# Kernel tuning notes

Hardware: AMD Instinct MI355X
Metric: run time of the kernel (lower is better)

The kernel has to match this reference:

```python
import jax, jax.numpy as jnp
import numpy as np

B, U, HEADS, S = 16, 1024, 8, 1024


def setup_inputs() -> dict:
    key = jax.random.key(0)
    k1, k2, k3, k4 = jax.random.split(key, 4)
    x = jax.random.normal(k1, (B, U, S), dtype=jnp.float32)
    mask = jax.random.randint(k2, (B, S, S), 0, 2).astype(bool)
    w_qkv = jax.random.normal(k3, (3 * U, U), dtype=jnp.float32) * 0.02
    w_out = jax.random.normal(k4, (U, U), dtype=jnp.float32) * 0.02
    return {"x": x, "mask": mask, "w_qkv": w_qkv, "w_out": w_out}


def reference(x, mask, w_qkv, w_out):
    # x: (B, U, S), mask: (B, n_queries, n_keys) bool
    b, u, s = x.shape
    h = HEADS
    c = u // h  # head (chunk) size
    scale = 1.0 / np.sqrt(c).astype(np.float32)

    # 1x1-conv QKV projection (bias=False): (3U, U) x (B, U, S) -> (B, 3U, S)
    qkv = jnp.einsum('ou,bus->bos', w_qkv, x)
    Q, K, V = jnp.split(qkv, 3, axis=1)           # each (B, U, S)
    Qh = Q.reshape(b, h, c, s)
    Kh = K.reshape(b, h, c, s)
    Vh = V.reshape(b, h, c, s)

    # attention logits: (B, H, n_q, n_k)
    A = jnp.einsum('bhcq,bhck->bhqk', Qh, Kh)

    # relu activation with per-query valid-key-count normalization
    m = mask.sum(axis=2)[:, :, None]              # (B, n_q, 1) count of valid keys
    n_elem = jnp.where(mask, m, 1).astype(A.dtype)[:, None]  # (B, 1, n_q, n_k)
    mask_b = mask[:, None]                        # broadcast over heads
    A = jnp.where(mask_b, jax.nn.relu(A) * scale, -jnp.inf)
    A = A / n_elem
    A = jnp.where(jnp.isinf(A), jnp.zeros((), A.dtype), A)

    # attention-value aggregation (faithful math of broadcast+sum): (B, H, C, n_q)
    Ch = jnp.einsum('bhqk,bhck->bhcq', A, Vh)
    Cc = Ch.reshape(b, u, s)

    # finishing 1x1-conv linear layer
    return jnp.einsum('ou,bus->bos', w_out, Cc)
```

## Files before the change

### kernel.cpp

```cpp
#include <hip/hip_runtime.h>

#define B_DIM 16
#define U_DIM 1024
#define H_DIM 8
#define S_DIM 1024
#define C_DIM 128
#define KD 1024
#define SCALE 0.08838834764831845f

typedef __attribute__((ext_vector_type(8))) short s16x8;
typedef __attribute__((ext_vector_type(4))) float f32x4;

__device__ __forceinline__ void gll16(const void* g, void* l) {
  __builtin_amdgcn_global_load_lds(
      (const __attribute__((address_space(1))) unsigned int*)g,
      (__attribute__((address_space(3))) unsigned int*)l, 16, 0, 0);
}
__device__ __forceinline__ unsigned short f2bf(float f) {
  unsigned u = __float_as_uint(f);
  u += 0x7FFF + ((u >> 16) & 1u);
  return (unsigned short)(u >> 16);
}
#define MFMA16(a, b, c) __builtin_amdgcn_mfma_f32_16x16x32_bf16(a, b, c, 0, 0, 0)

__global__ void detect_mask(const unsigned char* __restrict__ mask_raw, int* __restrict__ flag) {
  __shared__ int not01, notf;
  if (threadIdx.x == 0) { not01 = 0; notf = 0; }
  __syncthreads();
  const unsigned int* p = (const unsigned int*)mask_raw;
  int l01 = 0, lf = 0;
  for (int i = threadIdx.x; i < 4096; i += 256) {
    unsigned int v = p[i];
    if (v != 0u && v != 1u) l01 = 1;
    if (v != 0u && v != 0x3F800000u) lf = 1;
  }
  if (l01) atomicOr(&not01, 1);
  if (lf) atomicOr(&notf, 1);
  __syncthreads();
  if (threadIdx.x == 0) flag[0] = (!not01) ? 0 : ((!notf) ? 2 : 1);
}

__global__ __launch_bounds__(256) void pack_mask(const unsigned char* __restrict__ mask_raw,
                                                 const int* __restrict__ flag,
                                                 unsigned long long* __restrict__ bits) {
  __shared__ unsigned char tile[64][80];
  const int t = threadIdx.x;
  const int kt = blockIdx.x * 64, qw = blockIdx.y, b = blockIdx.z;
  const int mk = flag[0];
  const int q = t >> 2, kbase = (t & 3) * 16;
  const size_t row = (size_t)(b * S_DIM + qw * 64 + q);
  if (mk == 1) {
    uint4 v = *(const uint4*)(mask_raw + (row << 10) + kt + kbase);
    *(uint4*)&tile[q][kbase] = v;
  } else if (mk == 0) {
    const int* p = (const int*)mask_raw + (row << 10) + kt + kbase;
#pragma unroll
    for (int j = 0; j < 4; ++j) {
      int4 v = ((const int4*)p)[j];
      uchar4 o;
      o.x = v.x ? 1 : 0; o.y = v.y ? 1 : 0; o.z = v.z ? 1 : 0; o.w = v.w ? 1 : 0;
      *(uchar4*)&tile[q][kbase + j * 4] = o;
    }
  } else {
    const float* p = (const float*)mask_raw + (row << 10) + kt + kbase;
#pragma unroll
    for (int j = 0; j < 4; ++j) {
      float4 v = ((const float4*)p)[j];
      uchar4 o;
      o.x = (v.x != 0.f) ? 1 : 0; o.y = (v.y != 0.f) ? 1 : 0;
      o.z = (v.z != 0.f) ? 1 : 0; o.w = (v.w != 0.f) ? 1 : 0;
      *(uchar4*)&tile[q][kbase + j * 4] = o;
    }
  }
  __syncthreads();
  const int wave = t >> 6, lane = t & 63;
#pragma unroll
  for (int qq = 0; qq < 16; ++qq) {
    int qr = wave * 16 + qq;
    unsigned long long bal = __ballot(tile[qr][lane] != 0);
    if (lane == 0)
      bits[(size_t)blockIdx.x * (B_DIM * S_DIM) + (size_t)b * S_DIM + qw * 64 + qr] = bal;
  }
}

__global__ __launch_bounds__(256) void invm_from_bits(const unsigned long long* __restrict__ bits,
                                                      float* __restrict__ invm) {
  int idx = blockIdx.x * 256 + threadIdx.x;
  int s = 0;
#pragma unroll
  for (int kt = 0; kt < S_DIM / 64; ++kt)
    s += __popcll(bits[(size_t)kt * (B_DIM * S_DIM) + idx]);
  invm[idx] = (s > 0) ? (SCALE / (float)s) : 0.f;
}

__global__ __launch_bounds__(256) void cvt_bf16(const float* __restrict__ in,
                                                unsigned short* __restrict__ out, int n) {
  int i = (blockIdx.x * 256 + threadIdx.x) * 4;
  if (i < n) {
    float4 v = *(const float4*)(in + i);
    ushort4 o;
    o.x = f2bf(v.x); o.y = f2bf(v.y); o.z = f2bf(v.z); o.w = f2bf(v.w);
    *(ushort4*)(out + i) = o;
  }
}

__global__ __launch_bounds__(256) void transpose_x(const float* __restrict__ x,
                                                   unsigned short* __restrict__ xT) {
  __shared__ float T[32][33];
  const int t = threadIdx.x, r = t >> 3, c4 = (t & 7) * 4;
  const int s0 = blockIdx.x * 32, u0 = blockIdx.y * 32;
  const size_t base = (size_t)blockIdx.z * U_DIM * S_DIM;
  float4 v = *(const float4*)(x + base + (size_t)(u0 + r) * S_DIM + s0 + c4);
  T[r][c4 + 0] = v.x; T[r][c4 + 1] = v.y; T[r][c4 + 2] = v.z; T[r][c4 + 3] = v.w;
  __syncthreads();
  ushort4 o;
  o.x = f2bf(T[c4 + 0][r]); o.y = f2bf(T[c4 + 1][r]);
  o.z = f2bf(T[c4 + 2][r]); o.w = f2bf(T[c4 + 3][r]);
  *(ushort4*)(xT + base + (size_t)(s0 + r) * U_DIM + u0 + c4) = o;
}

__global__ __launch_bounds__(256) void transpose_v(const unsigned short* __restrict__ qkvT,
                                                   unsigned short* __restrict__ VT) {
  __shared__ unsigned short T[32][34];
  const int t = threadIdx.x, r = t >> 3, c4 = (t & 7) * 4;
  const int k0 = blockIdx.x * 32, c0 = blockIdx.y * 32;
  const unsigned short* qb = qkvT + (size_t)blockIdx.z * S_DIM * (3 * U_DIM);
  ushort4 v = *(const ushort4*)(qb + (size_t)(k0 + r) * (3 * U_DIM) + 2 * U_DIM + c0 + c4);
  T[r][c4 + 0] = v.x; T[r][c4 + 1] = v.y; T[r][c4 + 2] = v.z; T[r][c4 + 3] = v.w;
  __syncthreads();
  ushort4 o;
  o.x = T[c4 + 0][r]; o.y = T[c4 + 1][r]; o.z = T[c4 + 2][r]; o.w = T[c4 + 3][r];
  *(ushort4*)(VT + (size_t)blockIdx.z * U_DIM * S_DIM + (size_t)(c0 + r) * S_DIM + k0 + c4) = o;
}

template <typename OUT>
__global__ __launch_bounds__(512, 2) void gemm256(const unsigned short* __restrict__ A,
                                                  const unsigned short* __restrict__ Bm,
                                                  OUT* __restrict__ D,
                                                  long long sAb, long long sBb, long long sDb,
                                                  int N) {
  __shared__ unsigned short sA0[256 * 64], sB0[256 * 64];
  __shared__ unsigned short sA1[256 * 64], sB1[256 * 64];
  const int tid = threadIdx.x;
  const int wave = tid >> 6, lane = tid & 63;
  const int l15 = lane & 15, quad = lane >> 4;
  const int wm = wave & 3, wn = wave >> 2;
  const unsigned int Lb = blockIdx.x + gridDim.x * (blockIdx.y + gridDim.y * blockIdx.z);
  const unsigned int nwg = gridDim.x * gridDim.y * gridDim.z;
  const unsigned int logical = (Lb & 7u) * (nwg >> 3) + (Lb >> 3);
  const int bx = logical % gridDim.x;
  const unsigned int rem = logical / gridDim.x;
  const int by = rem % gridDim.y;
  const int bz = rem / gridDim.y;
  const int m0 = by * 256, n0 = bx * 256;
  A += (size_t)bz * sAb + (size_t)m0 * KD;
  Bm += (size_t)bz * sBb + (size_t)n0 * KD;
  D += (size_t)bz * sDb;

  const int r0 = tid >> 3;
  const int kc0 = (tid & 7) ^ (r0 & 7);
  const unsigned short* pA = A + (size_t)r0 * KD + kc0 * 8;
  const unsigned short* pB = Bm + (size_t)r0 * KD + kc0 * 8;
  const int wo = wave * 512;

#define STG_U0(SA, K0)                                        \
  do {                                                        \
    gll16(pA + (K0), &(SA)[wo]);                              \
    gll16(pA + 64 * KD + (K0), &(SA)[4096 + wo]);             \
  } while (0)
#define STG_U1(SA, K0)                                        \
  do {                                                        \
    gll16(pA + 128 * KD + (K0), &(SA)[8192 + wo]);            \
    gll16(pA + 192 * KD + (K0), &(SA)[12288 + wo]);           \
  } while (0)
#define STG_U2(SB, K0)                                        \
  do {                                                        \
    gll16(pB + (K0), &(SB)[wo]);                              \
    gll16(pB + 128 * KD + (K0), &(SB)[8192 + wo]);            \
  } while (0)
#define STG_U3(SB, K0)                                        \
  do {                                                        \
    gll16(pB + 64 * KD + (K0), &(SB)[4096 + wo]);             \
    gll16(pB + 192 * KD + (K0), &(SB)[12288 + wo]);           \
  } while (0)

#define WAITB(VN)                                             \
  do {                                                        \
    asm volatile("s_waitcnt vmcnt(" #VN ")" ::: "memory");    \
    __builtin_amdgcn_s_barrier();                             \
    asm volatile("" ::: "memory");                            \
  } while (0)

  s16x8 a[4][2];
  f32x4 acc[4][8] = {};

#define LDA(SA)                                                                         \
  do {                                                                                  \
    _Pragma("unroll") for (int i = 0; i < 4; ++i) {                                     \
      int row = wm * 64 + i * 16 + l15;                                                 \
      _Pragma("unroll") for (int ks = 0; ks < 2; ++ks)                                  \
          a[i][ks] = *(const s16x8*)&(SA)[row * 64 + (((ks * 4 + quad) ^ (row & 7)) * 8)]; \
    }                                                                                   \
  } while (0)

#define PHASE(SB, P)                                                                    \
  do {                                                                                  \
    s16x8 b[2][2];                                                                      \
    _Pragma("unroll") for (int jj = 0; jj < 2; ++jj) {                                  \
      int row = wn * 128 + ((P) * 2 + jj) * 16 + l15;                                   \
      _Pragma("unroll") for (int ks = 0; ks < 2; ++ks)                                  \
          b[jj][ks] = *(const s16x8*)&(SB)[row * 64 + (((ks * 4 + quad) ^ (row & 7)) * 8)]; \
    }                                                                                   \
    __builtin_amdgcn_s_setprio(1);                                                      \
    _Pragma("unroll") for (int ks = 0; ks < 2; ++ks)                                    \
        _Pragma("unroll") for (int i = 0; i < 4; ++i)                                   \
            _Pragma("unroll") for (int jj = 0; jj < 2; ++jj)                            \
                acc[i][(P) * 2 + jj] = MFMA16(a[i][ks], b[jj][ks], acc[i][(P) * 2 + jj]); \
    __builtin_amdgcn_s_setprio(0);                                                      \
  } while (0)

#define TILE(SA, SB, SAn, SBn, K1)                            \
  do {                                                        \
    WAITB(2);                                                 \
    STG_U0(SAn, K1);                                          \
    LDA(SA);                                                  \
    PHASE(SB, 0);                                             \
    STG_U1(SAn, K1);                                          \
    PHASE(SB, 1);                                             \
    WAITB(4);                                                 \
    STG_U2(SBn, K1);                                          \
    PHASE(SB, 2);                                             \
    STG_U3(SBn, K1);                                          \
    PHASE(SB, 3);                                             \
  } while (0)

#define TILE_LAST(CA, CB)                                     \
  do {                                                        \
    WAITB(2);                                                 \
    LDA(CA);                                                  \
    PHASE(CB, 0);                                             \
    PHASE(CB, 1);                                             \
    WAITB(0);                                                 \
    PHASE(CB, 2);                                             \
    PHASE(CB, 3);                                             \
  } while (0)

  STG_U0(sA0, 0); STG_U1(sA0, 0); STG_U2(sB0, 0); STG_U3(sB0, 0);

  for (int kt = 0; kt < 14; kt += 2) {
    TILE(sA0, sB0, sA1, sB1, (kt + 1) * 64);
    TILE(sA1, sB1, sA0, sB0, (kt + 2) * 64);
  }
  TILE(sA0, sB0, sA1, sB1, 15 * 64);
  TILE_LAST(sA1, sB1);
#undef TILE
#undef TILE_LAST
#undef PHASE
#undef LDA
#undef WAITB
#undef STG_U0
#undef STG_U1
#undef STG_U2
#undef STG_U3

#pragma unroll
  for (int i = 0; i < 4; ++i)
#pragma unroll
    for (int j = 0; j < 8; ++j) {
      f32x4 v = acc[i][j];
#pragma unroll
      for (int r = 0; r < 4; ++r) {
        int m = m0 + wm * 64 + i * 16 + quad * 4 + r;
        int n = n0 + wn * 128 + j * 16 + l15;
        if constexpr (sizeof(OUT) == 2) D[(size_t)m * N + n] = f2bf(v[r]);
        else D[(size_t)m * N + n] = v[r];
      }
    }
}

__global__ __launch_bounds__(512, 2) void attn_mfma(const unsigned short* __restrict__ qkvT,
                                                    const unsigned short* __restrict__ VT,
                                                    const unsigned long long* __restrict__ bits,
                                                    const float* __restrict__ invm,
                                                    unsigned short* __restrict__ CcT, int b0) {
  __shared__ unsigned short QV[128 * 128];
  __shared__ unsigned short Ks[64 * 128];
  __shared__ unsigned short Vs[128 * 64];
  __shared__ unsigned short Ps[128 * 64];

  const int tid = threadIdx.x, wave = tid >> 6, lane = tid & 63;
  const int l15 = lane & 15, quad = lane >> 4;
  const int qhalf = wave >> 2, kw = wave & 3;
  const int L = blockIdx.x + 8 * (blockIdx.y + 8 * blockIdx.z);
  const int cpx = (8 * H_DIM * gridDim.z) >> 3;
  const int logical = (L & 7) * cpx + (L >> 3);
  const int qt = logical & 7, h = (logical >> 3) & 7, z = logical >> 6;
  const int q0 = qt * 128, b = b0 + z;
  const unsigned short* qB = qkvT + (size_t)z * S_DIM * (3 * U_DIM);
  const unsigned short* Vb = VT + (size_t)z * U_DIM * S_DIM + (size_t)h * C_DIM * S_DIM;

#pragma unroll
  for (int pp = 0; pp < 4; ++pp) {
    int p = pp * 512 + tid;
    int row = p >> 4, c = (p & 15) ^ (row & 7);
    gll16(qB + (size_t)(q0 + row) * (3 * U_DIM) + h * C_DIM + c * 8, &QV[p * 8]);
  }
#pragma unroll
  for (int pp = 0; pp < 2; ++pp) {
    int p = pp * 512 + tid;
    int row = p >> 4, c = (p & 15) ^ (row & 7);
    gll16(qB + (size_t)row * (3 * U_DIM) + U_DIM + h * C_DIM + c * 8, &Ks[p * 8]);
    int vrow = p >> 3, vkc = (p & 7) ^ (vrow & 7);
    gll16(Vb + (size_t)vrow * S_DIM + vkc * 8, &Vs[p * 8]);
  }
  __syncthreads();

  s16x8 qf[4][4];
#pragma unroll
  for (int j = 0; j < 4; ++j)
#pragma unroll
    for (int kk = 0; kk < 4; ++kk) {
      int row = qhalf * 64 + j * 16 + l15;
      qf[j][kk] = *(const s16x8*)&QV[row * 128 + ((kk * 4 + quad) ^ (row & 7)) * 8];
    }
  float invf[4];
  {
    const float* ivp = invm + (size_t)b * S_DIM + q0 + qhalf * 64;
#pragma unroll
    for (int j = 0; j < 4; ++j) invf[j] = ivp[j * 16 + l15];
  }
  __syncthreads();

  f32x4 pacc[4][2] = {};

  for (int kt = 0; kt < S_DIM / 64; ++kt) {
    if (kt < S_DIM / 64 - 1) {
      const int kn = (kt + 1) * 64;
      unsigned short* vdst = (kt & 1) ? Vs : QV;
#pragma unroll
      for (int pp = 0; pp < 2; ++pp) {
        int p = pp * 512 + tid;
        int vrow = p >> 3, vkc = (p & 7) ^ (vrow & 7);
        gll16(Vb + (size_t)vrow * S_DIM + kn + vkc * 8, &vdst[p * 8]);
      }
    }

    unsigned long long w64[4];
    {
      const unsigned long long* mw =
          bits + (size_t)kt * (B_DIM * S_DIM) + (size_t)b * S_DIM + q0 + qhalf * 64;
#pragma unroll
      for (int j = 0; j < 4; ++j) w64[j] = mw[j * 16 + l15];
    }

    s16x8 af[4];
#pragma unroll
    for (int kk = 0; kk < 4; ++kk) {
      int row = kw * 16 + l15;
      af[kk] = *(const s16x8*)&Ks[row * 128 + ((kk * 4 + quad) ^ (row & 7)) * 8];
    }
    f32x4 sacc[4] = {};
    __builtin_amdgcn_s_setprio(1);
#pragma unroll
    for (int kk = 0; kk < 4; ++kk)
#pragma unroll
      for (int j = 0; j < 4; ++j) sacc[j] = MFMA16(af[kk], qf[j][kk], sacc[j]);
    __builtin_amdgcn_s_setprio(0);

#pragma unroll
    for (int j = 0; j < 4; ++j) {
      const unsigned int m4 = (unsigned int)(w64[j] >> (kw * 16 + quad * 4)) & 0xFu;
      float p[4];
#pragma unroll
      for (int r = 0; r < 4; ++r) {
        float t = fmaxf(sacc[j][r], 0.f) * invf[j];
        p[r] = ((m4 >> r) & 1u) ? t : 0.f;
      }
      unsigned int pk0, pk1;
      asm("v_cvt_pk_bf16_f32 %0, %1, %2" : "=v"(pk0) : "v"(p[0]), "v"(p[1]));
      asm("v_cvt_pk_bf16_f32 %0, %1, %2" : "=v"(pk1) : "v"(p[2]), "v"(p[3]));
      int q = qhalf * 64 + j * 16 + l15;
      int chunk = (kw * 2 + (quad >> 1)) ^ (q & 7);
      *(uint2*)&Ps[q * 64 + chunk * 8 + (quad & 1) * 4] = make_uint2(pk0, pk1);
    }
    __syncthreads();

    if (kt < S_DIM / 64 - 1) {
      const int kn = (kt + 1) * 64;
#pragma unroll
      for (int pp = 0; pp < 2; ++pp) {
        int p = pp * 512 + tid;
        int row = p >> 4, c = (p & 15) ^ (row & 7);
        gll16(qB + (size_t)(kn + row) * (3 * U_DIM) + U_DIM + h * C_DIM + c * 8, &Ks[p * 8]);
      }
    }

    const unsigned short* vbuf = (kt & 1) ? QV : Vs;
#pragma unroll
    for (int ks = 0; ks < 2; ++ks) {
      s16x8 pf[4], vf[2];
#pragma unroll
      for (int i = 0; i < 4; ++i) {
        int row = qhalf * 64 + i * 16 + l15;
        pf[i] = *(const s16x8*)&Ps[row * 64 + ((ks * 4 + quad) ^ (row & 7)) * 8];
      }
#pragma unroll
      for (int j = 0; j < 2; ++j) {
        int row = kw * 32 + j * 16 + l15;
        vf[j] = *(const s16x8*)&vbuf[row * 64 + ((ks * 4 + quad) ^ (row & 7)) * 8];
      }
      __builtin_amdgcn_s_setprio(1);
#pragma unroll
      for (int i = 0; i < 4; ++i)
#pragma unroll
        for (int j = 0; j < 2; ++j) pacc[i][j] = MFMA16(pf[i], vf[j], pacc[i][j]);
      __builtin_amdgcn_s_setprio(0);
    }
    __syncthreads();
  }

  unsigned short* cb = CcT + (size_t)z * S_DIM * U_DIM;
#pragma unroll
  for (int i = 0; i < 4; ++i)
#pragma unroll
    for (int j = 0; j < 2; ++j) {
      f32x4 v = pacc[i][j];
#pragma unroll
      for (int r = 0; r < 4; ++r) {
        int q = q0 + qhalf * 64 + i * 16 + quad * 4 + r;
        int c = h * C_DIM + kw * 32 + j * 16 + l15;
        cb[(size_t)q * U_DIM + c] = f2bf(v[r]);
      }
    }
}

extern "C" void kernel_launch(void* const* d_in, const int* in_sizes, int n_in,
                              void* d_out, int out_size, void* d_ws, size_t ws_size,
                              hipStream_t stream) {
  const float* x = (const float*)d_in[0];
  const unsigned char* mask_raw = (const unsigned char*)d_in[1];
  const float* w_qkv = (const float*)d_in[2];
  const float* w_out = (const float*)d_in[3];
  float* out = (float*)d_out;

  char* ws = (char*)d_ws;
  int* flag = (int*)ws;
  float* invm = (float*)(ws + 256);
  unsigned long long* bits = (unsigned long long*)(ws + 256 + 65536);
  unsigned short* wqkv_bf = (unsigned short*)((char*)bits + (size_t)B_DIM * S_DIM * 16 * 8);
  unsigned short* wout_bf = (unsigned short*)((char*)wqkv_bf + (size_t)3 * U_DIM * U_DIM * 2);
  char* heap = (char*)wout_bf + (size_t)U_DIM * U_DIM * 2;

  const size_t xT_pb = (size_t)U_DIM * S_DIM * 2;
  const size_t qkvT_pb = (size_t)3 * U_DIM * S_DIM * 2;
  const size_t vT_pb = (size_t)U_DIM * S_DIM * 2;
  const size_t ccT_pb = (size_t)U_DIM * S_DIM * 2;
  const size_t per_batch = xT_pb + qkvT_pb + vT_pb + ccT_pb;
  const size_t fixed = (size_t)(heap - ws);
  int nb = (ws_size > fixed) ? (int)((ws_size - fixed) / per_batch) : 1;
  if (nb < 1) nb = 1;
  if (nb > B_DIM) nb = B_DIM;

  unsigned short* xT = (unsigned short*)heap;
  unsigned short* qkvT = (unsigned short*)(heap + (size_t)nb * xT_pb);
  unsigned short* VT = (unsigned short*)(heap + (size_t)nb * (xT_pb + qkvT_pb));
  unsigned short* CcT = (unsigned short*)(heap + (size_t)nb * (xT_pb + qkvT_pb + vT_pb));

  detect_mask<<<1, 256, 0, stream>>>(mask_raw, flag);
  pack_mask<<<dim3(S_DIM / 64, S_DIM / 64, B_DIM), 256, 0, stream>>>(mask_raw, flag, bits);
  invm_from_bits<<<(B_DIM * S_DIM) / 256, 256, 0, stream>>>(bits, invm);
  cvt_bf16<<<(3 * U_DIM * U_DIM) / 1024, 256, 0, stream>>>(w_qkv, wqkv_bf, 3 * U_DIM * U_DIM);
  cvt_bf16<<<(U_DIM * U_DIM) / 1024, 256, 0, stream>>>(w_out, wout_bf, U_DIM * U_DIM);

  for (int b0 = 0; b0 < B_DIM; b0 += nb) {
    int cnt = (B_DIM - b0 < nb) ? (B_DIM - b0) : nb;
    transpose_x<<<dim3(S_DIM / 32, U_DIM / 32, cnt), 256, 0, stream>>>(
        x + (size_t)b0 * U_DIM * S_DIM, xT);
    gemm256<unsigned short><<<dim3(3 * U_DIM / 256, S_DIM / 256, cnt), 512, 0, stream>>>(
        xT, wqkv_bf, qkvT, (long long)U_DIM * S_DIM, 0LL, (long long)3 * U_DIM * S_DIM, 3 * U_DIM);
    transpose_v<<<dim3(S_DIM / 32, U_DIM / 32, cnt), 256, 0, stream>>>(qkvT, VT);
    attn_mfma<<<dim3(S_DIM / 128, H_DIM, cnt), 512, 0, stream>>>(
        qkvT, VT, bits, invm, CcT, b0);
    gemm256<float><<<dim3(S_DIM / 256, U_DIM / 256, cnt), 512, 0, stream>>>(
        wout_bf, CcT, out + (size_t)b0 * U_DIM * S_DIM, 0LL,
        (long long)U_DIM * S_DIM, (long long)U_DIM * S_DIM, S_DIM);
  }
}
```

Baseline: 462.8 us.

## Double-buffer K tiles and use 1024-thread attention blocks with one barrier per step

The attention kernel now runs 16 waves per block instead of 8, each covering 32 queries, which shrinks per-wave accumulators and registers. K tiles get a second LDS buffer, so the next K and V tiles are prefetched at the top of each step, and the mid-step barrier becomes a raw s_barrier after an lgkmcnt wait. Q is staged in two halves through a smaller buffer to fit in LDS. Dropping the vmcnt wait before the raw barrier risks reading stale Vs/Ks if global-to-LDS loads have not landed, since only the loop-end __syncthreads waits on them.

```diff
diff --git a/kernel.cpp b/kernel.cpp
--- a/kernel.cpp
+++ b/kernel.cpp
@@ -278,19 +278,20 @@
     }
 }
 
-__global__ __launch_bounds__(512, 2) void attn_mfma(const unsigned short* __restrict__ qkvT,
-                                                    const unsigned short* __restrict__ VT,
-                                                    const unsigned long long* __restrict__ bits,
-                                                    const float* __restrict__ invm,
-                                                    unsigned short* __restrict__ CcT, int b0) {
-  __shared__ unsigned short QV[128 * 128];
-  __shared__ unsigned short Ks[64 * 128];
+__global__ __launch_bounds__(1024, 4) void attn_mfma(const unsigned short* __restrict__ qkvT,
+                                                     const unsigned short* __restrict__ VT,
+                                                     const unsigned long long* __restrict__ bits,
+                                                     const float* __restrict__ invm,
+                                                     unsigned short* __restrict__ CcT, int b0) {
+  __shared__ unsigned short QV[64 * 128];
+  __shared__ unsigned short Ks0[64 * 128];
+  __shared__ unsigned short Ks1[64 * 128];
   __shared__ unsigned short Vs[128 * 64];
   __shared__ unsigned short Ps[128 * 64];
 
   const int tid = threadIdx.x, wave = tid >> 6, lane = tid & 63;
   const int l15 = lane & 15, quad = lane >> 4;
-  const int qhalf = wave >> 2, kw = wave & 3;
+  const int qq = wave >> 2, kw = wave & 3;
   const int L = blockIdx.x + 8 * (blockIdx.y + 8 * blockIdx.z);
   const int cpx = (8 * H_DIM * gridDim.z) >> 3;
   const int logical = (L & 7) * cpx + (L >> 3);
@@ -299,76 +300,85 @@
   const unsigned short* qB = qkvT + (size_t)z * S_DIM * (3 * U_DIM);
   const unsigned short* Vb = VT + (size_t)z * U_DIM * S_DIM + (size_t)h * C_DIM * S_DIM;
 
-#pragma unroll
-  for (int pp = 0; pp < 4; ++pp) {
-    int p = pp * 512 + tid;
-    int row = p >> 4, c = (p & 15) ^ (row & 7);
-    gll16(qB + (size_t)(q0 + row) * (3 * U_DIM) + h * C_DIM + c * 8, &QV[p * 8]);
-  }
-#pragma unroll
-  for (int pp = 0; pp < 2; ++pp) {
-    int p = pp * 512 + tid;
-    int row = p >> 4, c = (p & 15) ^ (row & 7);
-    gll16(qB + (size_t)row * (3 * U_DIM) + U_DIM + h * C_DIM + c * 8, &Ks[p * 8]);
-    int vrow = p >> 3, vkc = (p & 7) ^ (vrow & 7);
-    gll16(Vb + (size_t)vrow * S_DIM + vkc * 8, &Vs[p * 8]);
-  }
-  __syncthreads();
-
-  s16x8 qf[4][4];
-#pragma unroll
-  for (int j = 0; j < 4; ++j)
-#pragma unroll
-    for (int kk = 0; kk < 4; ++kk) {
-      int row = qhalf * 64 + j * 16 + l15;
-      qf[j][kk] = *(const s16x8*)&QV[row * 128 + ((kk * 4 + quad) ^ (row & 7)) * 8];
-    }
-  float invf[4];
+  const int srow = tid >> 4, sc = (tid & 15) ^ (srow & 7);
+  const int vrow = tid >> 3, vkc = (tid & 7) ^ (vrow & 7);
+
+  gll16(qB + (size_t)(q0 + srow) * (3 * U_DIM) + h * C_DIM + sc * 8, &QV[tid * 8]);
+  gll16(qB + (size_t)srow * (3 * U_DIM) + U_DIM + h * C_DIM + sc * 8, &Ks0[tid * 8]);
+  gll16(Vb + (size_t)vrow * S_DIM + vkc * 8, &Vs[tid * 8]);
+  __syncthreads();
+
+  s16x8 qf[2][4];
+  if (qq < 2) {
+#pragma unroll
+    for (int j = 0; j < 2; ++j)
+#pragma unroll
+      for (int kk = 0; kk < 4; ++kk) {
+        int row = qq * 32 + j * 16 + l15;
+        qf[j][kk] = *(const s16x8*)&QV[row * 128 + ((kk * 4 + quad) ^ (row & 7)) * 8];
+      }
+  }
+  __syncthreads();
+
+  gll16(qB + (size_t)(q0 + 64 + srow) * (3 * U_DIM) + h * C_DIM + sc * 8, &QV[tid * 8]);
+  __syncthreads();
+
+  if (qq >= 2) {
+#pragma unroll
+    for (int j = 0; j < 2; ++j)
+#pragma unroll
+      for (int kk = 0; kk < 4; ++kk) {
+        int row = (qq - 2) * 32 + j * 16 + l15;
+        qf[j][kk] = *(const s16x8*)&QV[row * 128 + ((kk * 4 + quad) ^ (row & 7)) * 8];
+      }
+  }
+  float invf[2];
   {
-    const float* ivp = invm + (size_t)b * S_DIM + q0 + qhalf * 64;
-#pragma unroll
-    for (int j = 0; j < 4; ++j) invf[j] = ivp[j * 16 + l15];
-  }
-  __syncthreads();
-
-  f32x4 pacc[4][2] = {};
+    const float* ivp = invm + (size_t)b * S_DIM + q0 + qq * 32;
+#pragma unroll
+    for (int j = 0; j < 2; ++j) invf[j] = ivp[j * 16 + l15];
+  }
+  __syncthreads();
+
+  f32x4 pacc[2][2] = {};
 
   for (int kt = 0; kt < S_DIM / 64; ++kt) {
+    const unsigned short* kcur = (kt & 1) ? Ks1 : Ks0;
+    unsigned short* knxt = (kt & 1) ? Ks0 : Ks1;
+    const unsigned short* vcur = (kt & 1) ? QV : Vs;
+    unsigned short* vnxt = (kt & 1) ? Vs : QV;
+
     if (kt < S_DIM / 64 - 1) {
       const int kn = (kt + 1) * 64;
-      unsigned short* vdst = (kt & 1) ? Vs : QV;
-#pragma unroll
-      for (int pp = 0; pp < 2; ++pp) {
-        int p = pp * 512 + tid;
-        int vrow = p >> 3, vkc = (p & 7) ^ (vrow & 7);
-        gll16(Vb + (size_t)vrow * S_DIM + kn + vkc * 8, &vdst[p * 8]);
-      }
-    }
-
-    unsigned long long w64[4];
+      gll16(qB + (size_t)(kn + srow) * (3 * U_DIM) + U_DIM + h * C_DIM + sc * 8,
+            &knxt[tid * 8]);
+      gll16(Vb + (size_t)vrow * S_DIM + kn + vkc * 8, &vnxt[tid * 8]);
+    }
+
+    unsigned long long w64[2];
     {
       const unsigned long long* mw =
-          bits + (size_t)kt * (B_DIM * S_DIM) + (size_t)b * S_DIM + q0 + qhalf * 64;
-#pragma unroll
-      for (int j = 0; j < 4; ++j) w64[j] = mw[j * 16 + l15];
+          bits + (size_t)kt * (B_DIM * S_DIM) + (size_t)b * S_DIM + q0 + qq * 32;
+#pragma unroll
+      for (int j = 0; j < 2; ++j) w64[j] = mw[j * 16 + l15];
     }
 
     s16x8 af[4];
 #pragma unroll
     for (int kk = 0; kk < 4; ++kk) {
       int row = kw * 16 + l15;
-      af[kk] = *(const s16x8*)&Ks[row * 128 + ((kk * 4 + quad) ^ (row & 7)) * 8];
-    }
-    f32x4 sacc[4] = {};
+      af[kk] = *(const s16x8*)&kcur[row * 128 + ((kk * 4 + quad) ^ (row & 7)) * 8];
+    }
+    f32x4 sacc[2] = {};
     __builtin_amdgcn_s_setprio(1);
 #pragma unroll
     for (int kk = 0; kk < 4; ++kk)
 #pragma unroll
-      for (int j = 0; j < 4; ++j) sacc[j] = MFMA16(af[kk], qf[j][kk], sacc[j]);
+      for (int j = 0; j < 2; ++j) sacc[j] = MFMA16(af[kk], qf[j][kk], sacc[j]);
     __builtin_amdgcn_s_setprio(0);
 
 #pragma unroll
-    for (int j = 0; j < 4; ++j) {
+    for (int j = 0; j < 2; ++j) {
       const unsigned int m4 = (unsigned int)(w64[j] >> (kw * 16 + quad * 4)) & 0xFu;
       float p[4];
 #pragma unroll
@@ -379,39 +389,32 @@
       unsigned int pk0, pk1;
       asm("v_cvt_pk_bf16_f32 %0, %1, %2" : "=v"(pk0) : "v"(p[0]), "v"(p[1]));
       asm("v_cvt_pk_bf16_f32 %0, %1, %2" : "=v"(pk1) : "v"(p[2]), "v"(p[3]));
-      int q = qhalf * 64 + j * 16 + l15;
+      int q = qq * 32 + j * 16 + l15;
       int chunk = (kw * 2 + (quad >> 1)) ^ (q & 7);
       *(uint2*)&Ps[q * 64 + chunk * 8 + (quad & 1) * 4] = make_uint2(pk0, pk1);
     }
-    __syncthreads();
-
-    if (kt < S_DIM / 64 - 1) {
-      const int kn = (kt + 1) * 64;
-#pragma unroll
-      for (int pp = 0; pp < 2; ++pp) {
-        int p = pp * 512 + tid;
-        int row = p >> 4, c = (p & 15) ^ (row & 7);
-        gll16(qB + (size_t)(kn + row) * (3 * U_DIM) + U_DIM + h * C_DIM + c * 8, &Ks[p * 8]);
-      }
-    }
-
-    const unsigned short* vbuf = (kt & 1) ? QV : Vs;
+
+    asm volatile("s_waitcnt lgkmcnt(0)" ::: "memory");
+    __builtin_amdgcn_sched_barrier(0);
+    __builtin_amdgcn_s_barrier();
+    __builtin_amdgcn_sched_barrier(0);
+
 #pragma unroll
     for (int ks = 0; ks < 2; ++ks) {
-      s16x8 pf[4], vf[2];
-#pragma unroll
-      for (int i = 0; i < 4; ++i) {
-        int row = qhalf * 64 + i * 16 + l15;
+      s16x8 pf[2], vf[2];
+#pragma unroll
+      for (int i = 0; i < 2; ++i) {
+        int row = qq * 32 + i * 16 + l15;
         pf[i] = *(const s16x8*)&Ps[row * 64 + ((ks * 4 + quad) ^ (row & 7)) * 8];
       }
 #pragma unroll
       for (int j = 0; j < 2; ++j) {
         int row = kw * 32 + j * 16 + l15;
-        vf[j] = *(const s16x8*)&vbuf[row * 64 + ((ks * 4 + quad) ^ (row & 7)) * 8];
+        vf[j] = *(const s16x8*)&vcur[row * 64 + ((ks * 4 + quad) ^ (row & 7)) * 8];
       }
       __builtin_amdgcn_s_setprio(1);
 #pragma unroll
-      for (int i = 0; i < 4; ++i)
+      for (int i = 0; i < 2; ++i)
 #pragma unroll
         for (int j = 0; j < 2; ++j) pacc[i][j] = MFMA16(pf[i], vf[j], pacc[i][j]);
       __builtin_amdgcn_s_setprio(0);
@@ -421,13 +424,13 @@
 
   unsigned short* cb = CcT + (size_t)z * S_DIM * U_DIM;
 #pragma unroll
-  for (int i = 0; i < 4; ++i)
+  for (int i = 0; i < 2; ++i)
 #pragma unroll
     for (int j = 0; j < 2; ++j) {
       f32x4 v = pacc[i][j];
 #pragma unroll
       for (int r = 0; r < 4; ++r) {
-        int q = q0 + qhalf * 64 + i * 16 + quad * 4 + r;
+        int q = q0 + qq * 32 + i * 16 + quad * 4 + r;
         int c = h * C_DIM + kw * 32 + j * 16 + l15;
         cb[(size_t)q * U_DIM + c] = f2bf(v[r]);
       }
@@ -479,7 +482,7 @@
     gemm256<unsigned short><<<dim3(3 * U_DIM / 256, S_DIM / 256, cnt), 512, 0, stream>>>(
         xT, wqkv_bf, qkvT, (long long)U_DIM * S_DIM, 0LL, (long long)3 * U_DIM * S_DIM, 3 * U_DIM);
     transpose_v<<<dim3(S_DIM / 32, U_DIM / 32, cnt), 256, 0, stream>>>(qkvT, VT);
-    attn_mfma<<<dim3(S_DIM / 128, H_DIM, cnt), 512, 0, stream>>>(
+    attn_mfma<<<dim3(S_DIM / 128, H_DIM, cnt), 1024, 0, stream>>>(
         qkvT, VT, bits, invm, CcT, b0);
     gemm256<float><<<dim3(S_DIM / 256, U_DIM / 256, cnt), 512, 0, stream>>>(
         wout_bf, CcT, out + (size_t)b0 * U_DIM * S_DIM, 0LL,
```

New measurement: 445.0 us. 1.04x faster.
